# Kernel tuning notes

Hardware: AMD Instinct MI355X
Metric: run time of the kernel (lower is better)

The kernel has to match this reference:

```python
import jax, jax.numpy as jnp
import numpy as np

N_LAYERS = 3


def _spmm(edge_val, edge_src, edge_dst, x, n_nodes):
    # sparse adjacency @ x via gather + segment-sum (COO SpMM)
    msgs = edge_val[:, None] * x[edge_src]          # [nnz, d]
    return jax.ops.segment_sum(msgs, edge_dst, num_segments=n_nodes)


def setup_inputs() -> dict:
    key = jax.random.key(0)
    ks = jax.random.split(key, 6)
    n_users, n_items, d, nnz, batch = 100000, 50000, 64, 4000000, 2048
    n_nodes = n_users + n_items
    return {
        "user_emb": jax.random.normal(ks[0], (n_users, d), jnp.float32) * 0.1,
        "item_emb": jax.random.normal(ks[1], (n_items, d), jnp.float32) * 0.1,
        "edge_val": jax.random.uniform(ks[2], (nnz,), jnp.float32),
        "edge_src": jax.random.randint(ks[3], (nnz,), 0, n_nodes, jnp.int32),
        "edge_dst": jax.random.randint(ks[4], (nnz,), 0, n_nodes, jnp.int32),
        "users": jax.random.randint(ks[5], (batch,), 0, n_users, jnp.int32),
    }


def reference(user_emb, item_emb, edge_val, edge_src, edge_dst, users):
    n_users = user_emb.shape[0]
    n_nodes = n_users + item_emb.shape[0]
    # LightGCN propagation: layer-0 embeddings + n_layers SpMM hops, mean over layers
    x = jnp.concatenate([user_emb, item_emb], axis=0)  # [N, d]
    acc = x
    for _ in range(N_LAYERS):
        x = _spmm(edge_val, edge_src, edge_dst, x, n_nodes)
        acc = acc + x
    light_out = acc / (N_LAYERS + 1)
    all_users = light_out[:n_users]
    all_items = light_out[n_users:]
    # get_user_rating: batch-user x all-item dot scoring
    users_emb = all_users[users]                      # [B, d]
    rating = jnp.matmul(users_emb, all_items.T)       # [B, n_items]
    return rating
```

## Files before the change

kernel.cpp:

```cpp
#include <hip/hip_runtime.h>

#define D 64
#define SCAN_BS 1024


__global__ void count_deg_kernel(const int* __restrict__ dst, int* __restrict__ counts, int nnz) {
    int e = blockIdx.x * blockDim.x + threadIdx.x;
    if (e < nnz) atomicAdd(&counts[dst[e]], 1);
}

__global__ void scan_blocks_kernel(const int* __restrict__ counts, int* __restrict__ offs,
                                   int* __restrict__ partials, int n) {
    __shared__ int sh[SCAN_BS];
    int tid = threadIdx.x;
    int i = blockIdx.x * SCAN_BS + tid;
    int v = (i < n) ? counts[i] : 0;
    sh[tid] = v;
    __syncthreads();
    for (int ofs = 1; ofs < SCAN_BS; ofs <<= 1) {
        int t = (tid >= ofs) ? sh[tid - ofs] : 0;
        __syncthreads();
        sh[tid] += t;
        __syncthreads();
    }
    if (i < n) offs[i] = sh[tid] - v;
    if (tid == SCAN_BS - 1) partials[blockIdx.x] = sh[tid];
}

__global__ void scan_partials_kernel(int* partials, int nb) {
    __shared__ int sh[SCAN_BS];
    int tid = threadIdx.x;
    int v = (tid < nb) ? partials[tid] : 0;
    sh[tid] = v;
    __syncthreads();
    for (int ofs = 1; ofs < SCAN_BS; ofs <<= 1) {
        int t = (tid >= ofs) ? sh[tid - ofs] : 0;
        __syncthreads();
        sh[tid] += t;
        __syncthreads();
    }
    if (tid < nb) partials[tid] = sh[tid] - v;
}

__global__ void add_base_kernel(int* __restrict__ offs, const int* __restrict__ partials,
                                int n, int nnz) {
    int i = blockIdx.x * SCAN_BS + threadIdx.x;
    if (i < n) offs[i] += partials[blockIdx.x];
    if (blockIdx.x == 0 && threadIdx.x == 0) offs[n] = nnz;
}

__global__ __launch_bounds__(256) void fill_csr_kernel(
        const int* __restrict__ src, const int* __restrict__ dst,
        const float* __restrict__ val, int* __restrict__ cursor,
        int2* __restrict__ csr, int nnz, int n_nodes) {
    int grp = blockIdx.x & 7;
    int blk = blockIdx.x >> 3;
    int nblk = (int)(gridDim.x >> 3);
    int lo = (int)(((long long)n_nodes * grp) >> 3);
    int hi = (int)(((long long)n_nodes * (grp + 1)) >> 3);
    int per = (nnz + nblk - 1) / nblk;
    int e_beg = blk * per;
    int e_end = min(nnz, e_beg + per);
    for (int e = e_beg + (int)threadIdx.x; e < e_end; e += 256) {
        int d = __builtin_nontemporal_load(&dst[e]);
        if (d >= lo && d < hi) {
            int p = atomicAdd(&cursor[d], 1);
            int2 pk = make_int2(__float_as_int(__builtin_nontemporal_load(&val[e])),
                                __builtin_nontemporal_load(&src[e]));
            csr[p] = pk;
        }
    }
}


template <bool FIRST, bool LAST>
__global__ __launch_bounds__(256) void spmm_kernel(
        const int* __restrict__ offs, const int2* __restrict__ csr,
        const float* __restrict__ x_in,
        const float* __restrict__ user_emb, const float* __restrict__ item_emb,
        float* __restrict__ x_out, float* __restrict__ acc,
        int n_nodes, int n_users) {
    int wave = (int)((blockIdx.x * blockDim.x + threadIdx.x) >> 6);
    if (wave >= n_nodes) return;
    int lane = threadIdx.x & 63;
    int g = lane >> 4;
    int sl = lane & 15;
    int e0 = offs[wave], e1 = offs[wave + 1];
    float4 s4 = make_float4(0.f, 0.f, 0.f, 0.f);
    for (int base = e0; base < e1; base += 64) {
        int e = base + lane;
        int2 pe = make_int2(0, 0);
        if (e < e1) pe = csr[e];
        int cnt = min(64, e1 - base);
        for (int j = 0; j < cnt; j += 4) {
            int jj = j + g;
            float vj = __shfl(__int_as_float(pe.x), jj);
            int sj = __shfl(pe.y, jj);
            const float* rp;
            if (FIRST)
                rp = (sj < n_users) ? (user_emb + (size_t)sj * D)
                                    : (item_emb + (size_t)(sj - n_users) * D);
            else
                rp = x_in + (size_t)sj * D;
            float4 r = ((const float4*)rp)[sl];
            s4.x = fmaf(vj, r.x, s4.x);
            s4.y = fmaf(vj, r.y, s4.y);
            s4.z = fmaf(vj, r.z, s4.z);
            s4.w = fmaf(vj, r.w, s4.w);
        }
    }
    s4.x += __shfl_xor(s4.x, 16); s4.x += __shfl_xor(s4.x, 32);
    s4.y += __shfl_xor(s4.y, 16); s4.y += __shfl_xor(s4.y, 32);
    s4.z += __shfl_xor(s4.z, 16); s4.z += __shfl_xor(s4.z, 32);
    s4.w += __shfl_xor(s4.w, 16); s4.w += __shfl_xor(s4.w, 32);
    if (lane < 16) {
        size_t oi = (size_t)wave * D + (size_t)sl * 4;
        float4 a = *(const float4*)(acc + oi);
        a.x += s4.x; a.y += s4.y; a.z += s4.z; a.w += s4.w;
        *(float4*)(acc + oi) = a;
        if (!LAST) *(float4*)(x_out + oi) = s4;
    }
}


#define BM 128
#define BN 128
#define TM 8
#define TN 8
#define KB 32
#define PAD 4

__global__ __launch_bounds__(256) void rating_gemm_kernel(
        const float* __restrict__ acc, const int* __restrict__ users,
        float* __restrict__ out, int n_users, int n_items, int batch) {
    __shared__ __align__(16) float As[KB][BM + PAD];
    __shared__ __align__(16) float Bs[KB][BN + PAD];
    int m0 = blockIdx.y * BM;
    int n0 = blockIdx.x * BN;
    int tid = threadIdx.x;
    int tx = tid & 15, ty = tid >> 4;
    float c[TM][TN] = {};

    for (int k0 = 0; k0 < D; k0 += KB) {
        for (int f = tid; f < BM * (KB / 4); f += 256) {
            int m = f >> 3;
            int k4 = (f & 7) * 4;
            float4 a = make_float4(0.f, 0.f, 0.f, 0.f);
            int gm = m0 + m;
            if (gm < batch) {
                int uid = users[gm];
                a = *(const float4*)(acc + (size_t)uid * D + k0 + k4);
            }
            As[k4 + 0][m] = a.x; As[k4 + 1][m] = a.y;
            As[k4 + 2][m] = a.z; As[k4 + 3][m] = a.w;
        }
        for (int f = tid; f < BN * (KB / 4); f += 256) {
            int n = f >> 3;
            int k4 = (f & 7) * 4;
            float4 b = make_float4(0.f, 0.f, 0.f, 0.f);
            int gi = n0 + n;
            if (gi < n_items) {
                b = *(const float4*)(acc + (size_t)(n_users + gi) * D + k0 + k4);
            }
            Bs[k4 + 0][n] = b.x; Bs[k4 + 1][n] = b.y;
            Bs[k4 + 2][n] = b.z; Bs[k4 + 3][n] = b.w;
        }
        __syncthreads();
        #pragma unroll
        for (int k = 0; k < KB; ++k) {
            float a[TM], b[TN];
            float4 t;
            t = *(const float4*)&As[k][ty * TM];     a[0] = t.x; a[1] = t.y; a[2] = t.z; a[3] = t.w;
            t = *(const float4*)&As[k][ty * TM + 4]; a[4] = t.x; a[5] = t.y; a[6] = t.z; a[7] = t.w;
            t = *(const float4*)&Bs[k][tx * TN];     b[0] = t.x; b[1] = t.y; b[2] = t.z; b[3] = t.w;
            t = *(const float4*)&Bs[k][tx * TN + 4]; b[4] = t.x; b[5] = t.y; b[6] = t.z; b[7] = t.w;
            #pragma unroll
            for (int i = 0; i < TM; ++i)
                #pragma unroll
                for (int j = 0; j < TN; ++j)
                    c[i][j] = fmaf(a[i], b[j], c[i][j]);
        }
        __syncthreads();
    }

    const float S = 1.0f / 16.0f;
    for (int i = 0; i < TM; ++i) {
        int m = m0 + ty * TM + i;
        if (m >= batch) break;
        float* row = out + (size_t)m * n_items;
        for (int j = 0; j < TN; j += 4) {
            int n = n0 + tx * TN + j;
            if (n + 4 <= n_items) {
                float4 v;
                v.x = c[i][j + 0] * S; v.y = c[i][j + 1] * S;
                v.z = c[i][j + 2] * S; v.w = c[i][j + 3] * S;
                *(float4*)(row + n) = v;
            } else {
                for (int u = 0; u < 4; ++u)
                    if (n + u < n_items) row[n + u] = c[i][j + u] * S;
            }
        }
    }
}


extern "C" void kernel_launch(void* const* d_in, const int* in_sizes, int n_in,
                              void* d_out, int out_size, void* d_ws, size_t ws_size,
                              hipStream_t stream) {
    const float* user_emb = (const float*)d_in[0];
    const float* item_emb = (const float*)d_in[1];
    const float* edge_val = (const float*)d_in[2];
    const int*   edge_src = (const int*)d_in[3];
    const int*   edge_dst = (const int*)d_in[4];
    const int*   users    = (const int*)d_in[5];

    const int n_users = in_sizes[0] / D;
    const int n_items = in_sizes[1] / D;
    const int nnz     = in_sizes[2];
    const int batch   = in_sizes[5];
    const int n_nodes = n_users + n_items;

    char* w = (char*)d_ws;
    size_t off = 0;
    auto alloc = [&](size_t bytes) -> void* {
        void* p = w + off;
        off += (bytes + 255) & ~(size_t)255;
        return p;
    };
    float* acc      = (float*)alloc((size_t)n_nodes * D * 4);
    float* xA       = (float*)alloc((size_t)n_nodes * D * 4);
    float* xB       = (float*)alloc((size_t)n_nodes * D * 4);
    int*   counts   = (int*)alloc((size_t)n_nodes * 4);
    int*   offs     = (int*)alloc((size_t)(n_nodes + 1) * 4);
    int*   partials = (int*)alloc((size_t)SCAN_BS * 4);
    int*   cursor   = (int*)alloc((size_t)n_nodes * 4);
    int2*  csr      = (int2*)alloc((size_t)nnz * 8);
    (void)ws_size; (void)n_in; (void)out_size;

    hipMemcpyAsync(acc, user_emb, (size_t)n_users * D * 4, hipMemcpyDeviceToDevice, stream);
    hipMemcpyAsync(acc + (size_t)n_users * D, item_emb, (size_t)n_items * D * 4,
                   hipMemcpyDeviceToDevice, stream);

    hipMemsetAsync(counts, 0, (size_t)n_nodes * 4, stream);
    count_deg_kernel<<<(nnz + 255) / 256, 256, 0, stream>>>(edge_dst, counts, nnz);
    int nb = (n_nodes + SCAN_BS - 1) / SCAN_BS;
    scan_blocks_kernel<<<nb, SCAN_BS, 0, stream>>>(counts, offs, partials, n_nodes);
    scan_partials_kernel<<<1, SCAN_BS, 0, stream>>>(partials, nb);
    add_base_kernel<<<nb, SCAN_BS, 0, stream>>>(offs, partials, n_nodes, nnz);
    hipMemcpyAsync(cursor, offs, (size_t)n_nodes * 4, hipMemcpyDeviceToDevice, stream);
    fill_csr_kernel<<<2048, 256, 0, stream>>>(edge_src, edge_dst, edge_val,
                                              cursor, csr, nnz, n_nodes);

    int spmm_blocks = (n_nodes + 3) / 4;
    spmm_kernel<true, false><<<spmm_blocks, 256, 0, stream>>>(
        offs, csr, nullptr, user_emb, item_emb, xA, acc, n_nodes, n_users);
    spmm_kernel<false, false><<<spmm_blocks, 256, 0, stream>>>(
        offs, csr, xA, nullptr, nullptr, xB, acc, n_nodes, n_users);
    spmm_kernel<false, true><<<spmm_blocks, 256, 0, stream>>>(
        offs, csr, xB, nullptr, nullptr, xA , acc, n_nodes, n_users);

    dim3 ggrid((n_items + BN - 1) / BN, (batch + BM - 1) / BM);
    rating_gemm_kernel<<<ggrid, 256, 0, stream>>>(acc, users, (float*)d_out,
                                                  n_users, n_items, batch);
}
```

Measured before the change: 1.408 ms.

## Defer layer accumulation to last SpMM and prefetch gathered rows

Drops the per-layer read-modify-write of the accumulator and the initial embedding copies into it. The last SpMM layer now sums the layer-0 embeddings, both earlier layer outputs and its own result, and writes that total to the accumulator. Each lane now handles two float4 values, so 8 edges are gathered per step instead of 4. The next edge's row is prefetched one step ahead to overlap gather latency. This costs more registers and extra reads in the last layer, in exchange for less total memory traffic.

```diff
diff --git a/kernel.cpp b/kernel.cpp
--- a/kernel.cpp
+++ b/kernel.cpp
@@ -78,47 +78,102 @@
         const int* __restrict__ offs, const int2* __restrict__ csr,
         const float* __restrict__ x_in,
         const float* __restrict__ user_emb, const float* __restrict__ item_emb,
-        float* __restrict__ x_out, float* __restrict__ acc,
+        const float* __restrict__ xp0, const float* __restrict__ xp1,
+        float* __restrict__ x_out,
         int n_nodes, int n_users) {
     int wave = (int)((blockIdx.x * blockDim.x + threadIdx.x) >> 6);
     if (wave >= n_nodes) return;
     int lane = threadIdx.x & 63;
-    int g = lane >> 4;
-    int sl = lane & 15;
+    int g = lane >> 3;
+    int sl = lane & 7;
     int e0 = offs[wave], e1 = offs[wave + 1];
-    float4 s4 = make_float4(0.f, 0.f, 0.f, 0.f);
+    float4 a0 = make_float4(0.f, 0.f, 0.f, 0.f);
+    float4 a1 = make_float4(0.f, 0.f, 0.f, 0.f);
+
     for (int base = e0; base < e1; base += 64) {
         int e = base + lane;
         int2 pe = make_int2(0, 0);
         if (e < e1) pe = csr[e];
         int cnt = min(64, e1 - base);
-        for (int j = 0; j < cnt; j += 4) {
-            int jj = j + g;
-            float vj = __shfl(__int_as_float(pe.x), jj);
-            int sj = __shfl(pe.y, jj);
+        float pv = __int_as_float(pe.x);
+        int   ps = pe.y;
+
+        float vc; float4 c0, c1;
+        {
+            int jj = g;
+            vc = __shfl(pv, jj);
+            int sj = __shfl(ps, jj);
             const float* rp;
             if (FIRST)
                 rp = (sj < n_users) ? (user_emb + (size_t)sj * D)
                                     : (item_emb + (size_t)(sj - n_users) * D);
             else
                 rp = x_in + (size_t)sj * D;
-            float4 r = ((const float4*)rp)[sl];
-            s4.x = fmaf(vj, r.x, s4.x);
-            s4.y = fmaf(vj, r.y, s4.y);
-            s4.z = fmaf(vj, r.z, s4.z);
-            s4.w = fmaf(vj, r.w, s4.w);
-        }
-    }
-    s4.x += __shfl_xor(s4.x, 16); s4.x += __shfl_xor(s4.x, 32);
-    s4.y += __shfl_xor(s4.y, 16); s4.y += __shfl_xor(s4.y, 32);
-    s4.z += __shfl_xor(s4.z, 16); s4.z += __shfl_xor(s4.z, 32);
-    s4.w += __shfl_xor(s4.w, 16); s4.w += __shfl_xor(s4.w, 32);
-    if (lane < 16) {
-        size_t oi = (size_t)wave * D + (size_t)sl * 4;
-        float4 a = *(const float4*)(acc + oi);
-        a.x += s4.x; a.y += s4.y; a.z += s4.z; a.w += s4.w;
-        *(float4*)(acc + oi) = a;
-        if (!LAST) *(float4*)(x_out + oi) = s4;
+            const float4* rq = (const float4*)rp;
+            c0 = rq[sl * 2];
+            c1 = rq[sl * 2 + 1];
+        }
+        for (int j = 0; j < cnt; j += 8) {
+            float vn = 0.f;
+            float4 n0 = make_float4(0.f, 0.f, 0.f, 0.f);
+            float4 n1 = make_float4(0.f, 0.f, 0.f, 0.f);
+            if (j + 8 < cnt) {
+                int jj = j + 8 + g;
+                vn = __shfl(pv, jj);
+                int sj = __shfl(ps, jj);
+                const float* rp;
+                if (FIRST)
+                    rp = (sj < n_users) ? (user_emb + (size_t)sj * D)
+                                        : (item_emb + (size_t)(sj - n_users) * D);
+                else
+                    rp = x_in + (size_t)sj * D;
+                const float4* rq = (const float4*)rp;
+                n0 = rq[sl * 2];
+                n1 = rq[sl * 2 + 1];
+            }
+            a0.x = fmaf(vc, c0.x, a0.x);
+            a0.y = fmaf(vc, c0.y, a0.y);
+            a0.z = fmaf(vc, c0.z, a0.z);
+            a0.w = fmaf(vc, c0.w, a0.w);
+            a1.x = fmaf(vc, c1.x, a1.x);
+            a1.y = fmaf(vc, c1.y, a1.y);
+            a1.z = fmaf(vc, c1.z, a1.z);
+            a1.w = fmaf(vc, c1.w, a1.w);
+            vc = vn; c0 = n0; c1 = n1;
+        }
+    }
+
+    a0.x += __shfl_xor(a0.x, 8);  a0.x += __shfl_xor(a0.x, 16); a0.x += __shfl_xor(a0.x, 32);
+    a0.y += __shfl_xor(a0.y, 8);  a0.y += __shfl_xor(a0.y, 16); a0.y += __shfl_xor(a0.y, 32);
+    a0.z += __shfl_xor(a0.z, 8);  a0.z += __shfl_xor(a0.z, 16); a0.z += __shfl_xor(a0.z, 32);
+    a0.w += __shfl_xor(a0.w, 8);  a0.w += __shfl_xor(a0.w, 16); a0.w += __shfl_xor(a0.w, 32);
+    a1.x += __shfl_xor(a1.x, 8);  a1.x += __shfl_xor(a1.x, 16); a1.x += __shfl_xor(a1.x, 32);
+    a1.y += __shfl_xor(a1.y, 8);  a1.y += __shfl_xor(a1.y, 16); a1.y += __shfl_xor(a1.y, 32);
+    a1.z += __shfl_xor(a1.z, 8);  a1.z += __shfl_xor(a1.z, 16); a1.z += __shfl_xor(a1.z, 32);
+    a1.w += __shfl_xor(a1.w, 8);  a1.w += __shfl_xor(a1.w, 16); a1.w += __shfl_xor(a1.w, 32);
+
+    if (lane < 8) {
+        size_t oi = (size_t)wave * D + (size_t)sl * 8;
+        if (LAST) {
+            const float* ep = (wave < n_users) ? (user_emb + (size_t)wave * D)
+                                               : (item_emb + (size_t)(wave - n_users) * D);
+            float4 z0 = ((const float4*)ep)[sl * 2];
+            float4 z1 = ((const float4*)ep)[sl * 2 + 1];
+            float4 y0 = *(const float4*)(xp0 + oi);
+            float4 y1 = *(const float4*)(xp0 + oi + 4);
+            float4 w0 = *(const float4*)(xp1 + oi);
+            float4 w1 = *(const float4*)(xp1 + oi + 4);
+            a0.x += z0.x + y0.x + w0.x;
+            a0.y += z0.y + y0.y + w0.y;
+            a0.z += z0.z + y0.z + w0.z;
+            a0.w += z0.w + y0.w + w0.w;
+            a1.x += z1.x + y1.x + w1.x;
+            a1.y += z1.y + y1.y + w1.y;
+            a1.z += z1.z + y1.z + w1.z;
+            a1.w += z1.w + y1.w + w1.w;
+        }
+        *(float4*)(x_out + oi) = a0;
+        *(float4*)(x_out + oi + 4) = a1;
     }
 }
 
@@ -237,10 +292,6 @@
     int2*  csr      = (int2*)alloc((size_t)nnz * 8);
     (void)ws_size; (void)n_in; (void)out_size;
 
-    hipMemcpyAsync(acc, user_emb, (size_t)n_users * D * 4, hipMemcpyDeviceToDevice, stream);
-    hipMemcpyAsync(acc + (size_t)n_users * D, item_emb, (size_t)n_items * D * 4,
-                   hipMemcpyDeviceToDevice, stream);
-
     hipMemsetAsync(counts, 0, (size_t)n_nodes * 4, stream);
     count_deg_kernel<<<(nnz + 255) / 256, 256, 0, stream>>>(edge_dst, counts, nnz);
     int nb = (n_nodes + SCAN_BS - 1) / SCAN_BS;
@@ -253,11 +304,11 @@
 
     int spmm_blocks = (n_nodes + 3) / 4;
     spmm_kernel<true, false><<<spmm_blocks, 256, 0, stream>>>(
-        offs, csr, nullptr, user_emb, item_emb, xA, acc, n_nodes, n_users);
+        offs, csr, nullptr, user_emb, item_emb, nullptr, nullptr, xA, n_nodes, n_users);
     spmm_kernel<false, false><<<spmm_blocks, 256, 0, stream>>>(
-        offs, csr, xA, nullptr, nullptr, xB, acc, n_nodes, n_users);
+        offs, csr, xA, nullptr, nullptr, nullptr, nullptr, xB, n_nodes, n_users);
     spmm_kernel<false, true><<<spmm_blocks, 256, 0, stream>>>(
-        offs, csr, xB, nullptr, nullptr, xA , acc, n_nodes, n_users);
+        offs, csr, xB, user_emb, item_emb, xA, xB, acc, n_nodes, n_users);
 
     dim3 ggrid((n_items + BN - 1) / BN, (batch + BM - 1) / BM);
     rating_gemm_kernel<<<ggrid, 256, 0, stream>>>(acc, users, (float*)d_out,
```

New measurement: 1.387 ms. Within noise of the previous version (-1.5%).
